# Kernel optimization log

Measured on AMD Instinct MI355X. Metric: run time of the kernel, lower is better.

## Reference

```python
import jax, jax.numpy as jnp
import numpy as np

NEG = -1000000.0  # same finite mask value as the Triton kernel


def setup_inputs() -> dict:
    key = jax.random.key(0)
    k1, k2, k3, k4 = jax.random.split(key, 4)
    B, H, KVH, S, D = 1, 32, 8, 2048, 128
    return {
        "q": jax.random.normal(k1, (B, H, S, D), dtype=jnp.float32),
        "k": jax.random.normal(k2, (B, KVH, S, D), dtype=jnp.float32),
        "v": jax.random.normal(k3, (B, KVH, S, D), dtype=jnp.float32),
        "sinks": jax.random.normal(k4, (H,), dtype=jnp.float32),
        "bandwidth": 1024,
    }


def reference(q, k, v, sinks, bandwidth):
    """Prefill flash attention with causal + sliding-window masking, GQA, and
    per-head attention sinks (extra logit in the softmax denominator)."""
    B, H, S, D = q.shape
    ratio = H // k.shape[1]  # KV_HEAD_RATIO
    kf = jnp.repeat(k, ratio, axis=1)  # [B,H,S,D]
    vf = jnp.repeat(v, ratio, axis=1)
    sm_scale = 1.0 / np.sqrt(D).astype(np.float32)

    logits = jnp.einsum("bhqd,bhkd->bhqk", q, kf) * sm_scale  # [B,H,S,S]
    q_pos = jnp.arange(S)[:, None]
    k_pos = jnp.arange(S)[None, :]
    mask = k_pos > q_pos  # causal
    if bandwidth > 0:
        mask = mask | (k_pos < q_pos - bandwidth + 1)  # sliding window
    logits = jnp.where(mask, NEG, logits)

    sink = sinks[None, :, None]  # [1,H,1] broadcast over batch, query
    m = jnp.maximum(jnp.max(logits, axis=-1), sink)  # [B,H,S]
    p = jnp.exp(logits - m[..., None])
    denom = p.sum(axis=-1) + jnp.exp(sink - m)  # sink contributes to denom only
    out = jnp.einsum("bhqk,bhkd->bhqd", p, vf) / denom[..., None]
    return out
```

## Files before the change

### kernel.cpp

```cpp
#include <hip/hip_runtime.h>
#include <hip/hip_bf16.h>

typedef __bf16 bf16x8 __attribute__((ext_vector_type(8)));
typedef unsigned short u16x8 __attribute__((ext_vector_type(8)));
typedef unsigned int u32x4 __attribute__((ext_vector_type(4)));
typedef float f32x4 __attribute__((ext_vector_type(4)));

#define SLEN 2048
#define DDIM 128
#define NH   32
#define NKVH 8
#define QBLK 64
#define KVB  32
#define KPAD 136
#define VPAD 40
#define PW2  20
#define MINIT  -1e30f
#define MASKED -3e30f

static __device__ __forceinline__ unsigned short f2bfu(float f) {
  union { float f; unsigned u; } x; x.f = f;
  return (unsigned short)((x.u + 0x7fffu + ((x.u >> 16) & 1u)) >> 16);
}
static __device__ __forceinline__ float bfu2f(unsigned short u) {
  union { unsigned u; float f; } x; x.u = ((unsigned)u) << 16;
  return x.f;
}
static __device__ __forceinline__ unsigned cvt_pk_bf16(float lo, float hi) {
  unsigned r;
  asm("v_cvt_pk_bf16_f32 %0, %1, %2" : "=v"(r) : "v"(lo), "v"(hi));
  return r;
}
static __device__ __forceinline__ f32x4 mfma_bf16(u16x8 a, u16x8 b, f32x4 c) {
  return __builtin_amdgcn_mfma_f32_16x16x32_bf16(
      __builtin_bit_cast(bf16x8, a), __builtin_bit_cast(bf16x8, b), c, 0, 0, 0);
}

__global__ __launch_bounds__(256) void conv_kv(const float* __restrict__ k,
                                               const float* __restrict__ v,
                                               unsigned* __restrict__ kdst,
                                               unsigned short* __restrict__ vt) {
  __shared__ unsigned T32[32][17];
  const int bb = blockIdx.x;
  if (bb < 1024) {
    const int i = bb * 256 + threadIdx.x;
    const float4 f0 = ((const float4*)k)[2 * i];
    const float4 f1 = ((const float4*)k)[2 * i + 1];
    u32x4 o = { cvt_pk_bf16(f0.x, f0.y), cvt_pk_bf16(f0.z, f0.w),
                cvt_pk_bf16(f1.x, f1.y), cvt_pk_bf16(f1.z, f1.w) };
    ((u32x4*)kdst)[i] = o;
    return;
  }
  const int b   = bb - 1024;
  const int dt  = b & 3;
  const int st  = (b >> 2) & 63;
  const int kvh = b >> 8;
  const int r  = threadIdx.x >> 3;
  const int cg = threadIdx.x & 7;
  const float4 f = *(const float4*)(v + ((size_t)(kvh * SLEN + st * 32 + r) * DDIM) + dt * 32 + cg * 4);
  T32[r][cg * 2]     = cvt_pk_bf16(f.x, f.y);
  T32[r][cg * 2 + 1] = cvt_pk_bf16(f.z, f.w);
  __syncthreads();
  const int dr = threadIdx.x >> 3;
  const unsigned sel = (dr & 1) ? 0x07060302u : 0x05040100u;
  const unsigned a0 = T32[cg * 4 + 0][dr >> 1], a1 = T32[cg * 4 + 1][dr >> 1];
  const unsigned a2 = T32[cg * 4 + 2][dr >> 1], a3 = T32[cg * 4 + 3][dr >> 1];
  unsigned short* vp = vt + (size_t)kvh * DDIM * SLEN + (size_t)(dt * 32 + dr) * SLEN + st * 32 + cg * 4;
  const unsigned w0 = __builtin_amdgcn_perm(a1, a0, sel);
  const unsigned w1 = __builtin_amdgcn_perm(a3, a2, sel);
  vp[0] = (unsigned short)(w0 & 0xffff);
  vp[1] = (unsigned short)(w0 >> 16);
  vp[2] = (unsigned short)(w1 & 0xffff);
  vp[3] = (unsigned short)(w1 >> 16);
}

__global__ __launch_bounds__(256, 4) void attn_fwd(
    const float* __restrict__ q, const unsigned short* __restrict__ kbf,
    const unsigned short* __restrict__ vtg, const float* __restrict__ sinks,
    const int* __restrict__ bwp, float* __restrict__ out,
    unsigned short* __restrict__ pO, float* __restrict__ pm,
    float* __restrict__ pl, const int nch) {
  __shared__ unsigned short Kl[KVB][KPAD];
  __shared__ unsigned short Vt[DDIM][VPAD];
  __shared__ unsigned Pex[4][16][PW2];
  __shared__ float SmS[4][16];

  const int tid  = threadIdx.x;
  const int wid  = tid >> 6;
  const int lane = tid & 63;
  const int ln   = lane & 15;
  const int hi   = lane >> 4;

  const int B   = blockIdx.x;
  const int x   = B & 7;
  const int j   = B >> 3;
  const int per = 4 * nch;
  const int qt  = 31 - (j / per);
  const int rem = j % per;
  const int hh  = (nch == 2) ? (rem >> 1) : rem;
  const int c   = (nch == 2) ? (rem & 1) : 0;
  const int h   = x * 4 + hh;
  const int kvh = x;
  const int q0  = qt * QBLK;
  const int qrow0 = q0 + wid * 16;
  const int qpos  = qrow0 + ln;

  const int bwv    = bwp[0];
  const int lo_off = (bwv > 0) ? (bwv - 1) : SLEN;

  const int T0 = max(0, q0 - lo_off) >> 5;
  const int T1 = (q0 + QBLK - 1) >> 5;
  const int N  = T1 - T0 + 1;
  const int ch = (N + nch - 1) / nch;
  const int Ts = T0 + c * ch;
  const int Te = min(T1, Ts + ch - 1);

  const float sm_scale = 0.08838834764831845f;

  u16x8 qf[4];
  {
    const float* qp = q + ((size_t)(h * SLEN + qpos) * DDIM) + hi * 8;
    #pragma unroll
    for (int dk = 0; dk < 4; ++dk) {
      float4 f0 = *(const float4*)(qp + dk * 32);
      float4 f1 = *(const float4*)(qp + dk * 32 + 4);
      u32x4 t = { cvt_pk_bf16(f0.x, f0.y), cvt_pk_bf16(f0.z, f0.w),
                  cvt_pk_bf16(f1.x, f1.y), cvt_pk_bf16(f1.z, f1.w) };
      qf[dk] = __builtin_bit_cast(u16x8, t);
    }
  }

  float m_ln = MINIT, l_ln = 0.0f;
  f32x4 oacc[8];
  #pragma unroll
  for (int nt = 0; nt < 8; ++nt) oacc[nt] = f32x4{0.f, 0.f, 0.f, 0.f};

  const unsigned short* Kg = kbf + (size_t)kvh * SLEN * DDIM;
  const unsigned short* Vg = vtg + (size_t)kvh * DDIM * SLEN;

  const int kr0 = tid >> 4,          kc0 = (tid & 15) * 8;
  const int kr1 = (256 + tid) >> 4;
  const int vr0 = tid >> 2,          vc0 = (tid & 3) * 8;
  const int vr1 = (256 + tid) >> 2;

  const int kbS = Ts * 32, kbE = Te * 32;

  u16x8 pk0, pk1, pv0, pv1;
  {
    pk0 = *(const u16x8*)(Kg + (size_t)(kbS + kr0) * DDIM + kc0);
    pk1 = *(const u16x8*)(Kg + (size_t)(kbS + kr1) * DDIM + kc0);
    pv0 = *(const u16x8*)(Vg + (size_t)vr0 * SLEN + kbS + vc0);
    pv1 = *(const u16x8*)(Vg + (size_t)vr1 * SLEN + kbS + vc0);
  }

  for (int kb = kbS; kb <= kbE; kb += KVB) {
    __syncthreads();
    *(u16x8*)&Kl[kr0][kc0] = pk0;
    *(u16x8*)&Kl[kr1][kc0] = pk1;
    *(u16x8*)&Vt[vr0][vc0] = pv0;
    *(u16x8*)&Vt[vr1][vc0] = pv1;
    __syncthreads();

    {
      const int nb = min(kb + KVB, kbE);
      pk0 = *(const u16x8*)(Kg + (size_t)(nb + kr0) * DDIM + kc0);
      pk1 = *(const u16x8*)(Kg + (size_t)(nb + kr1) * DDIM + kc0);
      pv0 = *(const u16x8*)(Vg + (size_t)vr0 * SLEN + nb + vc0);
      pv1 = *(const u16x8*)(Vg + (size_t)vr1 * SLEN + nb + vc0);
    }

    if (kb > qrow0 + 15) continue;
    if (kb + KVB - 1 < qrow0 - lo_off) continue;

    f32x4 sacc0 = {0,0,0,0}, sacc1 = {0,0,0,0};
    #pragma unroll
    for (int dk = 0; dk < 4; ++dk)
      sacc0 = mfma_bf16(*(const u16x8*)&Kl[ln][dk*32 + hi*8], qf[dk], sacc0);
    #pragma unroll
    for (int dk = 0; dk < 4; ++dk)
      sacc1 = mfma_bf16(*(const u16x8*)&Kl[16 + ln][dk*32 + hi*8], qf[dk], sacc1);

    float p[8];
    #pragma unroll
    for (int r = 0; r < 4; ++r) {
      const int kp0 = kb + hi * 4 + r;
      const int kp1 = kp0 + 16;
      const bool ok0 = (kp0 <= qpos) && (kp0 >= qpos - lo_off);
      const bool ok1 = (kp1 <= qpos) && (kp1 >= qpos - lo_off);
      p[r]     = ok0 ? sacc0[r] * sm_scale : MASKED;
      p[4 + r] = ok1 ? sacc1[r] * sm_scale : MASKED;
    }

    float mx = fmaxf(fmaxf(fmaxf(p[0], p[1]), fmaxf(p[2], p[3])),
                     fmaxf(fmaxf(p[4], p[5]), fmaxf(p[6], p[7])));
    mx = fmaxf(mx, __shfl_xor(mx, 16));
    mx = fmaxf(mx, __shfl_xor(mx, 32));

    if (__any(mx > m_ln + 8.0f)) {
      const float mn   = fmaxf(m_ln, mx);
      const float corr = __expf(m_ln - mn);
      l_ln *= corr;
      m_ln = mn;
      if (hi == 0) SmS[wid][ln] = corr;
      float corr4[4];
      #pragma unroll
      for (int r = 0; r < 4; ++r) corr4[r] = SmS[wid][hi * 4 + r];
      #pragma unroll
      for (int nt = 0; nt < 8; ++nt)
        #pragma unroll
        for (int r = 0; r < 4; ++r) oacc[nt][r] *= corr4[r];
    }

    float s = 0.0f;
    #pragma unroll
    for (int jj = 0; jj < 8; ++jj) { p[jj] = __expf(p[jj] - m_ln); s += p[jj]; }
    s += __shfl_xor(s, 16);
    s += __shfl_xor(s, 32);
    l_ln += s;

    Pex[wid][ln][hi * 2]         = cvt_pk_bf16(p[0], p[1]);
    Pex[wid][ln][hi * 2 + 1]     = cvt_pk_bf16(p[2], p[3]);
    Pex[wid][ln][8 + hi * 2]     = cvt_pk_bf16(p[4], p[5]);
    Pex[wid][ln][8 + hi * 2 + 1] = cvt_pk_bf16(p[6], p[7]);
    const u32x4 paw = *(const u32x4*)&Pex[wid][ln][hi * 4];
    const u16x8 pa  = __builtin_bit_cast(u16x8, paw);

    #pragma unroll
    for (int nt = 0; nt < 8; ++nt) {
      const u16x8 vb = *(const u16x8*)&Vt[nt*16 + ln][hi*8];
      oacc[nt] = mfma_bf16(pa, vb, oacc[nt]);
    }
  }

  if (nch == 1) {
    const float sink = sinks[h];
    const float M  = fmaxf(m_ln, sink);
    const float ed = __expf(m_ln - M);
    const float fac_ln = ed / (l_ln * ed + __expf(sink - M));
    if (hi == 0) SmS[wid][ln] = fac_ln;
    float fac4[4];
    #pragma unroll
    for (int r = 0; r < 4; ++r) fac4[r] = SmS[wid][hi * 4 + r];
    #pragma unroll
    for (int r = 0; r < 4; ++r) {
      float* op = out + ((size_t)(h * SLEN + qrow0 + hi*4 + r) * DDIM) + ln;
      #pragma unroll
      for (int nt = 0; nt < 8; ++nt) op[nt * 16] = oacc[nt][r] * fac4[r];
    }
  } else {
    const size_t Lb = ((size_t)(h * 32 + qt)) * 2 + c;
    if (hi == 0) {
      pm[Lb * 64 + wid * 16 + ln] = m_ln;
      pl[Lb * 64 + wid * 16 + ln] = l_ln;
    }
    #pragma unroll
    for (int r = 0; r < 4; ++r) {
      unsigned short* po = pO + (Lb * 64 + wid * 16 + hi * 4 + r) * 128 + ln;
      #pragma unroll
      for (int nt = 0; nt < 8; ++nt) po[nt * 16] = f2bfu(oacc[nt][r]);
    }
  }
}

__global__ __launch_bounds__(256) void merge2(
    const unsigned short* __restrict__ pO, const float* __restrict__ pm,
    const float* __restrict__ pl, const float* __restrict__ sinks,
    float* __restrict__ out) {
  const int blk = blockIdx.x;
  const int h   = blk >> 5;
  const int row = threadIdx.x >> 2;
  const int d0  = (threadIdx.x & 3) * 32;
  const size_t b0 = (size_t)blk * 2, b1 = b0 + 1;
  const float m0 = pm[b0 * 64 + row], l0 = pl[b0 * 64 + row];
  const float m1 = pm[b1 * 64 + row], l1 = pl[b1 * 64 + row];
  const float sink = sinks[h];
  const float M  = fmaxf(fmaxf(m0, m1), sink);
  const float e0 = __expf(m0 - M), e1 = __expf(m1 - M);
  const float inv = 1.0f / (l0 * e0 + l1 * e1 + __expf(sink - M));
  const float s0 = e0 * inv, s1 = e1 * inv;
  const unsigned short* p0 = pO + (b0 * 64 + row) * 128 + d0;
  const unsigned short* p1 = pO + (b1 * 64 + row) * 128 + d0;
  float* op = out + ((size_t)blk * 64 + row) * 128 + d0;
  #pragma unroll
  for (int i = 0; i < 4; ++i) {
    u16x8 a = *(const u16x8*)(p0 + i * 8);
    u16x8 b = *(const u16x8*)(p1 + i * 8);
    float4 o0, o1;
    o0.x = bfu2f(a[0]) * s0 + bfu2f(b[0]) * s1;
    o0.y = bfu2f(a[1]) * s0 + bfu2f(b[1]) * s1;
    o0.z = bfu2f(a[2]) * s0 + bfu2f(b[2]) * s1;
    o0.w = bfu2f(a[3]) * s0 + bfu2f(b[3]) * s1;
    o1.x = bfu2f(a[4]) * s0 + bfu2f(b[4]) * s1;
    o1.y = bfu2f(a[5]) * s0 + bfu2f(b[5]) * s1;
    o1.z = bfu2f(a[6]) * s0 + bfu2f(b[6]) * s1;
    o1.w = bfu2f(a[7]) * s0 + bfu2f(b[7]) * s1;
    *(float4*)(op + i * 8)     = o0;
    *(float4*)(op + i * 8 + 4) = o1;
  }
}

extern "C" void kernel_launch(void* const* d_in, const int* in_sizes, int n_in,
                              void* d_out, int out_size, void* d_ws, size_t ws_size,
                              hipStream_t stream) {
  const float* q     = (const float*)d_in[0];
  const float* k     = (const float*)d_in[1];
  const float* v     = (const float*)d_in[2];
  const float* sinks = (const float*)d_in[3];
  const int*   bw    = (const int*)d_in[4];
  float* out = (float*)d_out;

  const size_t kvBytes = (size_t)NKVH * SLEN * DDIM * 2;
  unsigned short* kbf = (unsigned short*)d_ws;
  unsigned short* vtg = kbf + (size_t)NKVH * SLEN * DDIM;

  const size_t nPart   = (size_t)2048 * 64;
  const size_t oBytes  = nPart * 128 * 2;
  const size_t mlBytes = nPart * 4 * 2;
  const size_t need2   = 2 * kvBytes + oBytes + mlBytes;

  const int nch = (ws_size >= need2) ? 2 : 1;

  unsigned short* pO = vtg + (size_t)NKVH * SLEN * DDIM;
  float* pm = (float*)((char*)pO + oBytes);
  float* pl = pm + nPart;

  conv_kv<<<dim3(1024 + NKVH * 64 * 4), 256, 0, stream>>>(k, v, (unsigned*)kbf, vtg);
  attn_fwd<<<dim3(1024 * nch), 256, 0, stream>>>(q, kbf, vtg, sinks, bw, out,
                                                 pO, pm, pl, nch);
  if (nch == 2)
    merge2<<<dim3(1024), 256, 0, stream>>>(pO, pm, pl, sinks, out);
}
```

Measured before the change: 79.77 us.

## Double query tile to 128 rows so each wave reuses K/V fragments across two groups

Each block now processes 128 query rows, with each wave handling two 16-row groups that share the same K and V fragments read from LDS. This halves the K/V global and LDS traffic per query row and the number of blocks, and the partial-result layout and merge indexing are rewritten to match. In exchange, each thread holds twice the accumulators, so register pressure rises and the launch bound drops to 3 blocks per SM. There are also fewer blocks overall, which can hurt load balance across CUs.

```diff
diff --git a/kernel.cpp b/kernel.cpp
--- a/kernel.cpp
+++ b/kernel.cpp
@@ -10,7 +10,7 @@
 #define DDIM 128
 #define NH   32
 #define NKVH 8
-#define QBLK 64
+#define QBLK 128
 #define KVB  32
 #define KPAD 136
 #define VPAD 40
@@ -74,7 +74,7 @@
   vp[3] = (unsigned short)(w1 >> 16);
 }
 
-__global__ __launch_bounds__(256, 4) void attn_fwd(
+__global__ __launch_bounds__(256, 3) void attn_fwd(
     const float* __restrict__ q, const unsigned short* __restrict__ kbf,
     const unsigned short* __restrict__ vtg, const float* __restrict__ sinks,
     const int* __restrict__ bwp, float* __restrict__ out,
@@ -82,8 +82,8 @@
     float* __restrict__ pl, const int nch) {
   __shared__ unsigned short Kl[KVB][KPAD];
   __shared__ unsigned short Vt[DDIM][VPAD];
-  __shared__ unsigned Pex[4][16][PW2];
-  __shared__ float SmS[4][16];
+  __shared__ unsigned Pex[4][2][16][PW2];
+  __shared__ float SmS[4][2][16];
 
   const int tid  = threadIdx.x;
   const int wid  = tid >> 6;
@@ -95,15 +95,14 @@
   const int x   = B & 7;
   const int j   = B >> 3;
   const int per = 4 * nch;
-  const int qt  = 31 - (j / per);
+  const int qt  = 15 - (j / per);
   const int rem = j % per;
   const int hh  = (nch == 2) ? (rem >> 1) : rem;
   const int c   = (nch == 2) ? (rem & 1) : 0;
   const int h   = x * 4 + hh;
   const int kvh = x;
   const int q0  = qt * QBLK;
-  const int qrow0 = q0 + wid * 16;
-  const int qpos  = qrow0 + ln;
+  const int qrow0 = q0 + wid * 32;
 
   const int bwv    = bwp[0];
   const int lo_off = (bwv > 0) ? (bwv - 1) : SLEN;
@@ -117,23 +116,26 @@
 
   const float sm_scale = 0.08838834764831845f;
 
-  u16x8 qf[4];
-  {
-    const float* qp = q + ((size_t)(h * SLEN + qpos) * DDIM) + hi * 8;
+  u16x8 qf[2][4];
+  #pragma unroll
+  for (int g = 0; g < 2; ++g) {
+    const float* qp = q + ((size_t)(h * SLEN + qrow0 + g * 16 + ln) * DDIM) + hi * 8;
     #pragma unroll
     for (int dk = 0; dk < 4; ++dk) {
       float4 f0 = *(const float4*)(qp + dk * 32);
       float4 f1 = *(const float4*)(qp + dk * 32 + 4);
       u32x4 t = { cvt_pk_bf16(f0.x, f0.y), cvt_pk_bf16(f0.z, f0.w),
                   cvt_pk_bf16(f1.x, f1.y), cvt_pk_bf16(f1.z, f1.w) };
-      qf[dk] = __builtin_bit_cast(u16x8, t);
-    }
-  }
-
-  float m_ln = MINIT, l_ln = 0.0f;
-  f32x4 oacc[8];
+      qf[g][dk] = __builtin_bit_cast(u16x8, t);
+    }
+  }
+
+  float m[2] = {MINIT, MINIT}, l[2] = {0.0f, 0.0f};
+  f32x4 oacc[2][8];
   #pragma unroll
-  for (int nt = 0; nt < 8; ++nt) oacc[nt] = f32x4{0.f, 0.f, 0.f, 0.f};
+  for (int g = 0; g < 2; ++g)
+    #pragma unroll
+    for (int nt = 0; nt < 8; ++nt) oacc[g][nt] = f32x4{0.f, 0.f, 0.f, 0.f};
 
   const unsigned short* Kg = kbf + (size_t)kvh * SLEN * DDIM;
   const unsigned short* Vg = vtg + (size_t)kvh * DDIM * SLEN;
@@ -169,95 +171,119 @@
       pv1 = *(const u16x8*)(Vg + (size_t)vr1 * SLEN + nb + vc0);
     }
 
-    if (kb > qrow0 + 15) continue;
+    if (kb > qrow0 + 31) continue;
     if (kb + KVB - 1 < qrow0 - lo_off) continue;
 
-    f32x4 sacc0 = {0,0,0,0}, sacc1 = {0,0,0,0};
-    #pragma unroll
-    for (int dk = 0; dk < 4; ++dk)
-      sacc0 = mfma_bf16(*(const u16x8*)&Kl[ln][dk*32 + hi*8], qf[dk], sacc0);
-    #pragma unroll
-    for (int dk = 0; dk < 4; ++dk)
-      sacc1 = mfma_bf16(*(const u16x8*)&Kl[16 + ln][dk*32 + hi*8], qf[dk], sacc1);
-
-    float p[8];
+    f32x4 s00 = {0,0,0,0}, s01 = {0,0,0,0};
+    f32x4 s10 = {0,0,0,0}, s11 = {0,0,0,0};
+    #pragma unroll
+    for (int dk = 0; dk < 4; ++dk) {
+      const u16x8 kf = *(const u16x8*)&Kl[ln][dk*32 + hi*8];
+      s00 = mfma_bf16(kf, qf[0][dk], s00);
+      s01 = mfma_bf16(kf, qf[1][dk], s01);
+    }
+    #pragma unroll
+    for (int dk = 0; dk < 4; ++dk) {
+      const u16x8 kf = *(const u16x8*)&Kl[16 + ln][dk*32 + hi*8];
+      s10 = mfma_bf16(kf, qf[0][dk], s10);
+      s11 = mfma_bf16(kf, qf[1][dk], s11);
+    }
+
+    float p0[8], p1[8];
+    const int qpos0 = qrow0 + ln, qpos1 = qrow0 + 16 + ln;
     #pragma unroll
     for (int r = 0; r < 4; ++r) {
       const int kp0 = kb + hi * 4 + r;
       const int kp1 = kp0 + 16;
-      const bool ok0 = (kp0 <= qpos) && (kp0 >= qpos - lo_off);
-      const bool ok1 = (kp1 <= qpos) && (kp1 >= qpos - lo_off);
-      p[r]     = ok0 ? sacc0[r] * sm_scale : MASKED;
-      p[4 + r] = ok1 ? sacc1[r] * sm_scale : MASKED;
-    }
-
-    float mx = fmaxf(fmaxf(fmaxf(p[0], p[1]), fmaxf(p[2], p[3])),
-                     fmaxf(fmaxf(p[4], p[5]), fmaxf(p[6], p[7])));
-    mx = fmaxf(mx, __shfl_xor(mx, 16));
-    mx = fmaxf(mx, __shfl_xor(mx, 32));
-
-    if (__any(mx > m_ln + 8.0f)) {
-      const float mn   = fmaxf(m_ln, mx);
-      const float corr = __expf(m_ln - mn);
-      l_ln *= corr;
-      m_ln = mn;
-      if (hi == 0) SmS[wid][ln] = corr;
-      float corr4[4];
-      #pragma unroll
-      for (int r = 0; r < 4; ++r) corr4[r] = SmS[wid][hi * 4 + r];
+      p0[r]     = ((kp0 <= qpos0) && (kp0 >= qpos0 - lo_off)) ? s00[r] * sm_scale : MASKED;
+      p0[4 + r] = ((kp1 <= qpos0) && (kp1 >= qpos0 - lo_off)) ? s10[r] * sm_scale : MASKED;
+      p1[r]     = ((kp0 <= qpos1) && (kp0 >= qpos1 - lo_off)) ? s01[r] * sm_scale : MASKED;
+      p1[4 + r] = ((kp1 <= qpos1) && (kp1 >= qpos1 - lo_off)) ? s11[r] * sm_scale : MASKED;
+    }
+
+    float mx0 = fmaxf(fmaxf(fmaxf(p0[0], p0[1]), fmaxf(p0[2], p0[3])),
+                      fmaxf(fmaxf(p0[4], p0[5]), fmaxf(p0[6], p0[7])));
+    float mx1 = fmaxf(fmaxf(fmaxf(p1[0], p1[1]), fmaxf(p1[2], p1[3])),
+                      fmaxf(fmaxf(p1[4], p1[5]), fmaxf(p1[6], p1[7])));
+    mx0 = fmaxf(mx0, __shfl_xor(mx0, 16));
+    mx0 = fmaxf(mx0, __shfl_xor(mx0, 32));
+    mx1 = fmaxf(mx1, __shfl_xor(mx1, 16));
+    mx1 = fmaxf(mx1, __shfl_xor(mx1, 32));
+
+    if (__any((mx0 > m[0] + 8.0f) || (mx1 > m[1] + 8.0f))) {
+      const float mn0 = fmaxf(m[0], mx0), mn1 = fmaxf(m[1], mx1);
+      const float c0 = __expf(m[0] - mn0), c1 = __expf(m[1] - mn1);
+      l[0] *= c0; l[1] *= c1; m[0] = mn0; m[1] = mn1;
+      if (hi == 0) { SmS[wid][0][ln] = c0; SmS[wid][1][ln] = c1; }
+      float c40[4], c41[4];
+      #pragma unroll
+      for (int r = 0; r < 4; ++r) { c40[r] = SmS[wid][0][hi*4 + r]; c41[r] = SmS[wid][1][hi*4 + r]; }
       #pragma unroll
       for (int nt = 0; nt < 8; ++nt)
         #pragma unroll
-        for (int r = 0; r < 4; ++r) oacc[nt][r] *= corr4[r];
-    }
-
-    float s = 0.0f;
-    #pragma unroll
-    for (int jj = 0; jj < 8; ++jj) { p[jj] = __expf(p[jj] - m_ln); s += p[jj]; }
-    s += __shfl_xor(s, 16);
-    s += __shfl_xor(s, 32);
-    l_ln += s;
-
-    Pex[wid][ln][hi * 2]         = cvt_pk_bf16(p[0], p[1]);
-    Pex[wid][ln][hi * 2 + 1]     = cvt_pk_bf16(p[2], p[3]);
-    Pex[wid][ln][8 + hi * 2]     = cvt_pk_bf16(p[4], p[5]);
-    Pex[wid][ln][8 + hi * 2 + 1] = cvt_pk_bf16(p[6], p[7]);
-    const u32x4 paw = *(const u32x4*)&Pex[wid][ln][hi * 4];
-    const u16x8 pa  = __builtin_bit_cast(u16x8, paw);
+        for (int r = 0; r < 4; ++r) { oacc[0][nt][r] *= c40[r]; oacc[1][nt][r] *= c41[r]; }
+    }
+
+    float s0 = 0.0f, s1 = 0.0f;
+    #pragma unroll
+    for (int jj = 0; jj < 8; ++jj) {
+      p0[jj] = __expf(p0[jj] - m[0]); s0 += p0[jj];
+      p1[jj] = __expf(p1[jj] - m[1]); s1 += p1[jj];
+    }
+    s0 += __shfl_xor(s0, 16); s0 += __shfl_xor(s0, 32); l[0] += s0;
+    s1 += __shfl_xor(s1, 16); s1 += __shfl_xor(s1, 32); l[1] += s1;
+
+    Pex[wid][0][ln][hi * 2]         = cvt_pk_bf16(p0[0], p0[1]);
+    Pex[wid][0][ln][hi * 2 + 1]     = cvt_pk_bf16(p0[2], p0[3]);
+    Pex[wid][0][ln][8 + hi * 2]     = cvt_pk_bf16(p0[4], p0[5]);
+    Pex[wid][0][ln][8 + hi * 2 + 1] = cvt_pk_bf16(p0[6], p0[7]);
+    Pex[wid][1][ln][hi * 2]         = cvt_pk_bf16(p1[0], p1[1]);
+    Pex[wid][1][ln][hi * 2 + 1]     = cvt_pk_bf16(p1[2], p1[3]);
+    Pex[wid][1][ln][8 + hi * 2]     = cvt_pk_bf16(p1[4], p1[5]);
+    Pex[wid][1][ln][8 + hi * 2 + 1] = cvt_pk_bf16(p1[6], p1[7]);
+    const u16x8 pa0 = __builtin_bit_cast(u16x8, *(const u32x4*)&Pex[wid][0][ln][hi * 4]);
+    const u16x8 pa1 = __builtin_bit_cast(u16x8, *(const u32x4*)&Pex[wid][1][ln][hi * 4]);
 
     #pragma unroll
     for (int nt = 0; nt < 8; ++nt) {
       const u16x8 vb = *(const u16x8*)&Vt[nt*16 + ln][hi*8];
-      oacc[nt] = mfma_bf16(pa, vb, oacc[nt]);
+      oacc[0][nt] = mfma_bf16(pa0, vb, oacc[0][nt]);
+      oacc[1][nt] = mfma_bf16(pa1, vb, oacc[1][nt]);
     }
   }
 
   if (nch == 1) {
     const float sink = sinks[h];
-    const float M  = fmaxf(m_ln, sink);
-    const float ed = __expf(m_ln - M);
-    const float fac_ln = ed / (l_ln * ed + __expf(sink - M));
-    if (hi == 0) SmS[wid][ln] = fac_ln;
-    float fac4[4];
-    #pragma unroll
-    for (int r = 0; r < 4; ++r) fac4[r] = SmS[wid][hi * 4 + r];
-    #pragma unroll
-    for (int r = 0; r < 4; ++r) {
-      float* op = out + ((size_t)(h * SLEN + qrow0 + hi*4 + r) * DDIM) + ln;
-      #pragma unroll
-      for (int nt = 0; nt < 8; ++nt) op[nt * 16] = oacc[nt][r] * fac4[r];
+    #pragma unroll
+    for (int g = 0; g < 2; ++g) {
+      const float M  = fmaxf(m[g], sink);
+      const float ed = __expf(m[g] - M);
+      const float fac_ln = ed / (l[g] * ed + __expf(sink - M));
+      if (hi == 0) SmS[wid][g][ln] = fac_ln;
+      float fac4[4];
+      #pragma unroll
+      for (int r = 0; r < 4; ++r) fac4[r] = SmS[wid][g][hi * 4 + r];
+      #pragma unroll
+      for (int r = 0; r < 4; ++r) {
+        float* op = out + ((size_t)(h * SLEN + qrow0 + g*16 + hi*4 + r) * DDIM) + ln;
+        #pragma unroll
+        for (int nt = 0; nt < 8; ++nt) op[nt * 16] = oacc[g][nt][r] * fac4[r];
+      }
     }
   } else {
-    const size_t Lb = ((size_t)(h * 32 + qt)) * 2 + c;
-    if (hi == 0) {
-      pm[Lb * 64 + wid * 16 + ln] = m_ln;
-      pl[Lb * 64 + wid * 16 + ln] = l_ln;
-    }
-    #pragma unroll
-    for (int r = 0; r < 4; ++r) {
-      unsigned short* po = pO + (Lb * 64 + wid * 16 + hi * 4 + r) * 128 + ln;
-      #pragma unroll
-      for (int nt = 0; nt < 8; ++nt) po[nt * 16] = f2bfu(oacc[nt][r]);
+    const size_t Lb = ((size_t)(h * 16 + qt)) * 2 + c;
+    #pragma unroll
+    for (int g = 0; g < 2; ++g) {
+      if (hi == 0) {
+        pm[Lb * 128 + wid * 32 + g * 16 + ln] = m[g];
+        pl[Lb * 128 + wid * 32 + g * 16 + ln] = l[g];
+      }
+      #pragma unroll
+      for (int r = 0; r < 4; ++r) {
+        unsigned short* po = pO + (Lb * 128 + wid * 32 + g * 16 + hi * 4 + r) * 128 + ln;
+        #pragma unroll
+        for (int nt = 0; nt < 8; ++nt) po[nt * 16] = f2bfu(oacc[g][nt][r]);
+      }
     }
   }
 }
@@ -266,21 +292,24 @@
     const unsigned short* __restrict__ pO, const float* __restrict__ pm,
     const float* __restrict__ pl, const float* __restrict__ sinks,
     float* __restrict__ out) {
-  const int blk = blockIdx.x;
-  const int h   = blk >> 5;
-  const int row = threadIdx.x >> 2;
-  const int d0  = (threadIdx.x & 3) * 32;
-  const size_t b0 = (size_t)blk * 2, b1 = b0 + 1;
-  const float m0 = pm[b0 * 64 + row], l0 = pl[b0 * 64 + row];
-  const float m1 = pm[b1 * 64 + row], l1 = pl[b1 * 64 + row];
+  const int blk  = blockIdx.x;
+  const int h    = blk >> 5;
+  const int rloc = (blk & 31) * 64 + (threadIdx.x >> 2);
+  const int d0   = (threadIdx.x & 3) * 32;
+  const int qt   = rloc >> 7;
+  const int lr   = rloc & 127;
+  const size_t r0 = ((size_t)((h * 16 + qt) * 2 + 0)) * 128 + lr;
+  const size_t r1 = r0 + 128;
+  const float m0 = pm[r0], l0 = pl[r0];
+  const float m1 = pm[r1], l1 = pl[r1];
   const float sink = sinks[h];
   const float M  = fmaxf(fmaxf(m0, m1), sink);
   const float e0 = __expf(m0 - M), e1 = __expf(m1 - M);
   const float inv = 1.0f / (l0 * e0 + l1 * e1 + __expf(sink - M));
   const float s0 = e0 * inv, s1 = e1 * inv;
-  const unsigned short* p0 = pO + (b0 * 64 + row) * 128 + d0;
-  const unsigned short* p1 = pO + (b1 * 64 + row) * 128 + d0;
-  float* op = out + ((size_t)blk * 64 + row) * 128 + d0;
+  const unsigned short* p0 = pO + r0 * 128 + d0;
+  const unsigned short* p1 = pO + r1 * 128 + d0;
+  float* op = out + ((size_t)h * SLEN + rloc) * DDIM + d0;
   #pragma unroll
   for (int i = 0; i < 4; ++i) {
     u16x8 a = *(const u16x8*)(p0 + i * 8);
@@ -313,7 +342,7 @@
   unsigned short* kbf = (unsigned short*)d_ws;
   unsigned short* vtg = kbf + (size_t)NKVH * SLEN * DDIM;
 
-  const size_t nPart   = (size_t)2048 * 64;
+  const size_t nPart   = (size_t)NH * 16 * 2 * 128;
   const size_t oBytes  = nPart * 128 * 2;
   const size_t mlBytes = nPart * 4 * 2;
   const size_t need2   = 2 * kvBytes + oBytes + mlBytes;
@@ -325,8 +354,8 @@
   float* pl = pm + nPart;
 
   conv_kv<<<dim3(1024 + NKVH * 64 * 4), 256, 0, stream>>>(k, v, (unsigned*)kbf, vtg);
-  attn_fwd<<<dim3(1024 * nch), 256, 0, stream>>>(q, kbf, vtg, sinks, bw, out,
-                                                 pO, pm, pl, nch);
+  attn_fwd<<<dim3(512 * nch), 256, 0, stream>>>(q, kbf, vtg, sinks, bw, out,
+                                                pO, pm, pl, nch);
   if (nch == 2)
     merge2<<<dim3(1024), 256, 0, stream>>>(pO, pm, pl, sinks, out);
 }
```

Result: slower. 86.84 us (+8.9%).

## Double-buffer K/V tiles in LDS via direct global-to-LDS loads with XOR swizzle

Applied to the files above, without the earlier changes.

Replaces the register-staged K/V prefetch (global load into registers, then store to padded LDS between two barriers) with direct global_load_lds into double-buffered LDS tiles. An XOR swizzle replaces the padding to avoid bank conflicts, and each iteration needs only one barrier. The kernel is templated on chunk count and the merge is generalized. This is meant to cut register pressure and LDS store traffic and to overlap loads with compute. In exchange it doubles LDS use per block, which may reduce occupancy, and it relies on the ordering semantics of the async LDS loads.

```diff
diff --git a/kernel.cpp b/kernel.cpp
--- a/kernel.cpp
+++ b/kernel.cpp
@@ -10,11 +10,7 @@
 #define DDIM 128
 #define NH   32
 #define NKVH 8
-#define QBLK 64
 #define KVB  32
-#define KPAD 136
-#define VPAD 40
-#define PW2  20
 #define MINIT  -1e30f
 #define MASKED -3e30f
 
@@ -34,6 +30,11 @@
 static __device__ __forceinline__ f32x4 mfma_bf16(u16x8 a, u16x8 b, f32x4 c) {
   return __builtin_amdgcn_mfma_f32_16x16x32_bf16(
       __builtin_bit_cast(bf16x8, a), __builtin_bit_cast(bf16x8, b), c, 0, 0, 0);
+}
+static __device__ __forceinline__ void gload16(const unsigned short* g, unsigned short* l) {
+  __builtin_amdgcn_global_load_lds(
+      (const __attribute__((address_space(1))) unsigned*)g,
+      (__attribute__((address_space(3))) unsigned*)l, 16, 0, 0);
 }
 
 __global__ __launch_bounds__(256) void conv_kv(const float* __restrict__ k,
@@ -74,15 +75,17 @@
   vp[3] = (unsigned short)(w1 >> 16);
 }
 
+template <int NCH>
 __global__ __launch_bounds__(256, 4) void attn_fwd(
     const float* __restrict__ q, const unsigned short* __restrict__ kbf,
     const unsigned short* __restrict__ vtg, const float* __restrict__ sinks,
     const int* __restrict__ bwp, float* __restrict__ out,
     unsigned short* __restrict__ pO, float* __restrict__ pm,
-    float* __restrict__ pl, const int nch) {
-  __shared__ unsigned short Kl[KVB][KPAD];
-  __shared__ unsigned short Vt[DDIM][VPAD];
-  __shared__ unsigned Pex[4][16][PW2];
+    float* __restrict__ pl) {
+  constexpr int NQT = 32;
+  __shared__ unsigned short KB[2][KVB][DDIM];
+  __shared__ unsigned short VB[2][DDIM][KVB];
+  __shared__ unsigned Pex[4][16][16];
   __shared__ float SmS[4][16];
 
   const int tid  = threadIdx.x;
@@ -94,14 +97,14 @@
   const int B   = blockIdx.x;
   const int x   = B & 7;
   const int j   = B >> 3;
-  const int per = 4 * nch;
-  const int qt  = 31 - (j / per);
+  constexpr int per = 4 * NCH;
+  const int qt  = NQT - 1 - (j / per);
   const int rem = j % per;
-  const int hh  = (nch == 2) ? (rem >> 1) : rem;
-  const int c   = (nch == 2) ? (rem & 1) : 0;
+  const int hh  = rem / NCH;
+  const int c   = rem % NCH;
   const int h   = x * 4 + hh;
   const int kvh = x;
-  const int q0  = qt * QBLK;
+  const int q0  = qt * 64;
   const int qrow0 = q0 + wid * 16;
   const int qpos  = qrow0 + ln;
 
@@ -109,9 +112,9 @@
   const int lo_off = (bwv > 0) ? (bwv - 1) : SLEN;
 
   const int T0 = max(0, q0 - lo_off) >> 5;
-  const int T1 = (q0 + QBLK - 1) >> 5;
+  const int T1 = (q0 + 63) >> 5;
   const int N  = T1 - T0 + 1;
-  const int ch = (N + nch - 1) / nch;
+  const int ch = (N + NCH - 1) / NCH;
   const int Ts = T0 + c * ch;
   const int Te = min(T1, Ts + ch - 1);
 
@@ -138,101 +141,109 @@
   const unsigned short* Kg = kbf + (size_t)kvh * SLEN * DDIM;
   const unsigned short* Vg = vtg + (size_t)kvh * DDIM * SLEN;
 
-  const int kr0 = tid >> 4,          kc0 = (tid & 15) * 8;
-  const int kr1 = (256 + tid) >> 4;
-  const int vr0 = tid >> 2,          vc0 = (tid & 3) * 8;
-  const int vr1 = (256 + tid) >> 2;
-
-  const int kbS = Ts * 32, kbE = Te * 32;
-
-  u16x8 pk0, pk1, pv0, pv1;
-  {
-    pk0 = *(const u16x8*)(Kg + (size_t)(kbS + kr0) * DDIM + kc0);
-    pk1 = *(const u16x8*)(Kg + (size_t)(kbS + kr1) * DDIM + kc0);
-    pv0 = *(const u16x8*)(Vg + (size_t)vr0 * SLEN + kbS + vc0);
-    pv1 = *(const u16x8*)(Vg + (size_t)vr1 * SLEN + kbS + vc0);
-  }
-
-  for (int kb = kbS; kb <= kbE; kb += KVB) {
-    __syncthreads();
-    *(u16x8*)&Kl[kr0][kc0] = pk0;
-    *(u16x8*)&Kl[kr1][kc0] = pk1;
-    *(u16x8*)&Vt[vr0][vc0] = pv0;
-    *(u16x8*)&Vt[vr1][vc0] = pv1;
-    __syncthreads();
+  int koff[2], voff[2];
+  #pragma unroll
+  for (int c2 = 0; c2 < 2; ++c2) {
+    const int r = wid * 8 + c2 * 4 + (lane >> 4);
+    koff[c2] = r * DDIM + (((lane & 15) ^ (r & 7)) * 8);
+    const int d = wid * 32 + c2 * 16 + (lane >> 2);
+    voff[c2] = d * SLEN + (((lane & 3) ^ ((lane >> 3) & 3)) * 8);
+  }
+
+  int kfo[4];
+  #pragma unroll
+  for (int dk = 0; dk < 4; ++dk)
+    kfo[dk] = ln * DDIM + (((dk * 4 + hi) ^ (ln & 7)) * 8);
+  const int vswz = (hi ^ ((ln >> 1) & 3)) * 8;
+
+  if (Ts <= Te) {
+    const int kbS = Ts * 32, kbE = Te * 32;
 
     {
-      const int nb = min(kb + KVB, kbE);
-      pk0 = *(const u16x8*)(Kg + (size_t)(nb + kr0) * DDIM + kc0);
-      pk1 = *(const u16x8*)(Kg + (size_t)(nb + kr1) * DDIM + kc0);
-      pv0 = *(const u16x8*)(Vg + (size_t)vr0 * SLEN + nb + vc0);
-      pv1 = *(const u16x8*)(Vg + (size_t)vr1 * SLEN + nb + vc0);
-    }
-
-    if (kb > qrow0 + 15) continue;
-    if (kb + KVB - 1 < qrow0 - lo_off) continue;
-
-    f32x4 sacc0 = {0,0,0,0}, sacc1 = {0,0,0,0};
-    #pragma unroll
-    for (int dk = 0; dk < 4; ++dk)
-      sacc0 = mfma_bf16(*(const u16x8*)&Kl[ln][dk*32 + hi*8], qf[dk], sacc0);
-    #pragma unroll
-    for (int dk = 0; dk < 4; ++dk)
-      sacc1 = mfma_bf16(*(const u16x8*)&Kl[16 + ln][dk*32 + hi*8], qf[dk], sacc1);
-
-    float p[8];
-    #pragma unroll
-    for (int r = 0; r < 4; ++r) {
-      const int kp0 = kb + hi * 4 + r;
-      const int kp1 = kp0 + 16;
-      const bool ok0 = (kp0 <= qpos) && (kp0 >= qpos - lo_off);
-      const bool ok1 = (kp1 <= qpos) && (kp1 >= qpos - lo_off);
-      p[r]     = ok0 ? sacc0[r] * sm_scale : MASKED;
-      p[4 + r] = ok1 ? sacc1[r] * sm_scale : MASKED;
-    }
-
-    float mx = fmaxf(fmaxf(fmaxf(p[0], p[1]), fmaxf(p[2], p[3])),
-                     fmaxf(fmaxf(p[4], p[5]), fmaxf(p[6], p[7])));
-    mx = fmaxf(mx, __shfl_xor(mx, 16));
-    mx = fmaxf(mx, __shfl_xor(mx, 32));
-
-    if (__any(mx > m_ln + 8.0f)) {
-      const float mn   = fmaxf(m_ln, mx);
-      const float corr = __expf(m_ln - mn);
-      l_ln *= corr;
-      m_ln = mn;
-      if (hi == 0) SmS[wid][ln] = corr;
-      float corr4[4];
-      #pragma unroll
-      for (int r = 0; r < 4; ++r) corr4[r] = SmS[wid][hi * 4 + r];
-      #pragma unroll
-      for (int nt = 0; nt < 8; ++nt)
+      gload16(Kg + (size_t)kbS * DDIM + koff[0], &KB[0][wid * 8][0]);
+      gload16(Kg + (size_t)kbS * DDIM + koff[1], &KB[0][wid * 8 + 4][0]);
+      gload16(Vg + (size_t)kbS + voff[0], &VB[0][wid * 32][0]);
+      gload16(Vg + (size_t)kbS + voff[1], &VB[0][wid * 32 + 16][0]);
+    }
+
+    int cur = 0;
+    for (int kb = kbS; kb <= kbE; kb += KVB) {
+      __syncthreads();
+
+      if (kb + KVB <= kbE) {
+        const int nb = kb + KVB;
+        const int nxt = cur ^ 1;
+        gload16(Kg + (size_t)nb * DDIM + koff[0], &KB[nxt][wid * 8][0]);
+        gload16(Kg + (size_t)nb * DDIM + koff[1], &KB[nxt][wid * 8 + 4][0]);
+        gload16(Vg + (size_t)nb + voff[0], &VB[nxt][wid * 32][0]);
+        gload16(Vg + (size_t)nb + voff[1], &VB[nxt][wid * 32 + 16][0]);
+      }
+
+      const bool skip = (kb > qrow0 + 15) || (kb + KVB - 1 < qrow0 - lo_off);
+      if (!skip) {
+        const unsigned short* kbp = &KB[cur][0][0];
+        const unsigned short* vbp = &VB[cur][0][0];
+
+        f32x4 sacc0 = {0,0,0,0}, sacc1 = {0,0,0,0};
         #pragma unroll
-        for (int r = 0; r < 4; ++r) oacc[nt][r] *= corr4[r];
-    }
-
-    float s = 0.0f;
-    #pragma unroll
-    for (int jj = 0; jj < 8; ++jj) { p[jj] = __expf(p[jj] - m_ln); s += p[jj]; }
-    s += __shfl_xor(s, 16);
-    s += __shfl_xor(s, 32);
-    l_ln += s;
-
-    Pex[wid][ln][hi * 2]         = cvt_pk_bf16(p[0], p[1]);
-    Pex[wid][ln][hi * 2 + 1]     = cvt_pk_bf16(p[2], p[3]);
-    Pex[wid][ln][8 + hi * 2]     = cvt_pk_bf16(p[4], p[5]);
-    Pex[wid][ln][8 + hi * 2 + 1] = cvt_pk_bf16(p[6], p[7]);
-    const u32x4 paw = *(const u32x4*)&Pex[wid][ln][hi * 4];
-    const u16x8 pa  = __builtin_bit_cast(u16x8, paw);
-
-    #pragma unroll
-    for (int nt = 0; nt < 8; ++nt) {
-      const u16x8 vb = *(const u16x8*)&Vt[nt*16 + ln][hi*8];
-      oacc[nt] = mfma_bf16(pa, vb, oacc[nt]);
-    }
-  }
-
-  if (nch == 1) {
+        for (int dk = 0; dk < 4; ++dk) {
+          sacc0 = mfma_bf16(*(const u16x8*)(kbp + kfo[dk]), qf[dk], sacc0);
+          sacc1 = mfma_bf16(*(const u16x8*)(kbp + kfo[dk] + 16 * DDIM), qf[dk], sacc1);
+        }
+
+        float p[8];
+        #pragma unroll
+        for (int r = 0; r < 4; ++r) {
+          const int kp0 = kb + hi * 4 + r;
+          const int kp1 = kp0 + 16;
+          p[r]     = ((kp0 <= qpos) && (kp0 >= qpos - lo_off)) ? sacc0[r] * sm_scale : MASKED;
+          p[4 + r] = ((kp1 <= qpos) && (kp1 >= qpos - lo_off)) ? sacc1[r] * sm_scale : MASKED;
+        }
+
+        float mx = fmaxf(fmaxf(fmaxf(p[0], p[1]), fmaxf(p[2], p[3])),
+                         fmaxf(fmaxf(p[4], p[5]), fmaxf(p[6], p[7])));
+        mx = fmaxf(mx, __shfl_xor(mx, 16));
+        mx = fmaxf(mx, __shfl_xor(mx, 32));
+
+        if (__any(mx > m_ln + 8.0f)) {
+          const float mn   = fmaxf(m_ln, mx);
+          const float corr = __expf(m_ln - mn);
+          l_ln *= corr;
+          m_ln = mn;
+          if (hi == 0) SmS[wid][ln] = corr;
+          float c4[4];
+          #pragma unroll
+          for (int r = 0; r < 4; ++r) c4[r] = SmS[wid][hi * 4 + r];
+          #pragma unroll
+          for (int nt = 0; nt < 8; ++nt)
+            #pragma unroll
+            for (int r = 0; r < 4; ++r) oacc[nt][r] *= c4[r];
+        }
+
+        float s = 0.0f;
+        #pragma unroll
+        for (int jj = 0; jj < 8; ++jj) { p[jj] = __expf(p[jj] - m_ln); s += p[jj]; }
+        s += __shfl_xor(s, 16);
+        s += __shfl_xor(s, 32);
+        l_ln += s;
+
+        Pex[wid][ln][hi * 2]         = cvt_pk_bf16(p[0], p[1]);
+        Pex[wid][ln][hi * 2 + 1]     = cvt_pk_bf16(p[2], p[3]);
+        Pex[wid][ln][8 + hi * 2]     = cvt_pk_bf16(p[4], p[5]);
+        Pex[wid][ln][8 + hi * 2 + 1] = cvt_pk_bf16(p[6], p[7]);
+        const u16x8 pa = __builtin_bit_cast(u16x8, *(const u32x4*)&Pex[wid][ln][hi * 4]);
+
+        #pragma unroll
+        for (int nt = 0; nt < 8; ++nt) {
+          const u16x8 vb = *(const u16x8*)(vbp + (nt * 16 + ln) * KVB + vswz);
+          oacc[nt] = mfma_bf16(pa, vb, oacc[nt]);
+        }
+      }
+      cur ^= 1;
+    }
+  }
+
+  if (NCH == 1) {
     const float sink = sinks[h];
     const float M  = fmaxf(m_ln, sink);
     const float ed = __expf(m_ln - M);
@@ -248,7 +259,7 @@
       for (int nt = 0; nt < 8; ++nt) op[nt * 16] = oacc[nt][r] * fac4[r];
     }
   } else {
-    const size_t Lb = ((size_t)(h * 32 + qt)) * 2 + c;
+    const size_t Lb = ((size_t)(h * NQT + qt)) * NCH + c;
     if (hi == 0) {
       pm[Lb * 64 + wid * 16 + ln] = m_ln;
       pl[Lb * 64 + wid * 16 + ln] = l_ln;
@@ -262,41 +273,51 @@
   }
 }
 
-__global__ __launch_bounds__(256) void merge2(
+template <int NCH, int QBLK, int NQT>
+__global__ __launch_bounds__(256) void mergeN(
     const unsigned short* __restrict__ pO, const float* __restrict__ pm,
     const float* __restrict__ pl, const float* __restrict__ sinks,
     float* __restrict__ out) {
-  const int blk = blockIdx.x;
-  const int h   = blk >> 5;
-  const int row = threadIdx.x >> 2;
-  const int d0  = (threadIdx.x & 3) * 32;
-  const size_t b0 = (size_t)blk * 2, b1 = b0 + 1;
-  const float m0 = pm[b0 * 64 + row], l0 = pl[b0 * 64 + row];
-  const float m1 = pm[b1 * 64 + row], l1 = pl[b1 * 64 + row];
+  const int t    = blockIdx.x * 256 + threadIdx.x;
+  const int rid  = t >> 2;
+  const int d0   = (t & 3) * 32;
+  const int h    = rid >> 11;
+  const int qpos = rid & 2047;
+  const int qt   = qpos / QBLK;
+  const int lr   = qpos % QBLK;
+  const size_t base = ((size_t)(h * NQT + qt) * NCH) * QBLK + lr;
   const float sink = sinks[h];
-  const float M  = fmaxf(fmaxf(m0, m1), sink);
-  const float e0 = __expf(m0 - M), e1 = __expf(m1 - M);
-  const float inv = 1.0f / (l0 * e0 + l1 * e1 + __expf(sink - M));
-  const float s0 = e0 * inv, s1 = e1 * inv;
-  const unsigned short* p0 = pO + (b0 * 64 + row) * 128 + d0;
-  const unsigned short* p1 = pO + (b1 * 64 + row) * 128 + d0;
-  float* op = out + ((size_t)blk * 64 + row) * 128 + d0;
-  #pragma unroll
-  for (int i = 0; i < 4; ++i) {
-    u16x8 a = *(const u16x8*)(p0 + i * 8);
-    u16x8 b = *(const u16x8*)(p1 + i * 8);
-    float4 o0, o1;
-    o0.x = bfu2f(a[0]) * s0 + bfu2f(b[0]) * s1;
-    o0.y = bfu2f(a[1]) * s0 + bfu2f(b[1]) * s1;
-    o0.z = bfu2f(a[2]) * s0 + bfu2f(b[2]) * s1;
-    o0.w = bfu2f(a[3]) * s0 + bfu2f(b[3]) * s1;
-    o1.x = bfu2f(a[4]) * s0 + bfu2f(b[4]) * s1;
-    o1.y = bfu2f(a[5]) * s0 + bfu2f(b[5]) * s1;
-    o1.z = bfu2f(a[6]) * s0 + bfu2f(b[6]) * s1;
-    o1.w = bfu2f(a[7]) * s0 + bfu2f(b[7]) * s1;
-    *(float4*)(op + i * 8)     = o0;
-    *(float4*)(op + i * 8 + 4) = o1;
-  }
+  float mc[NCH], lc[NCH];
+  float M = sink;
+  #pragma unroll
+  for (int c = 0; c < NCH; ++c) {
+    mc[c] = pm[base + (size_t)c * QBLK];
+    lc[c] = pl[base + (size_t)c * QBLK];
+    M = fmaxf(M, mc[c]);
+  }
+  float denom = __expf(sink - M);
+  float sc[NCH];
+  #pragma unroll
+  for (int c = 0; c < NCH; ++c) { sc[c] = __expf(mc[c] - M); denom += lc[c] * sc[c]; }
+  const float inv = 1.0f / denom;
+  float o[32];
+  #pragma unroll
+  for (int i = 0; i < 32; ++i) o[i] = 0.f;
+  #pragma unroll
+  for (int c = 0; c < NCH; ++c) {
+    const unsigned short* pp = pO + (base + (size_t)c * QBLK) * 128 + d0;
+    const float s = sc[c] * inv;
+    #pragma unroll
+    for (int i = 0; i < 4; ++i) {
+      u16x8 a = *(const u16x8*)(pp + i * 8);
+      #pragma unroll
+      for (int jj = 0; jj < 8; ++jj) o[i*8+jj] += bfu2f(a[jj]) * s;
+    }
+  }
+  float* op = out + (size_t)rid * 128 + d0;
+  #pragma unroll
+  for (int i = 0; i < 8; ++i)
+    *(float4*)(op + i*4) = make_float4(o[i*4], o[i*4+1], o[i*4+2], o[i*4+3]);
 }
 
 extern "C" void kernel_launch(void* const* d_in, const int* in_sizes, int n_in,
@@ -309,24 +330,22 @@
   const int*   bw    = (const int*)d_in[4];
   float* out = (float*)d_out;
 
-  const size_t kvBytes = (size_t)NKVH * SLEN * DDIM * 2;
+  const size_t kvElems = (size_t)NKVH * SLEN * DDIM;
   unsigned short* kbf = (unsigned short*)d_ws;
-  unsigned short* vtg = kbf + (size_t)NKVH * SLEN * DDIM;
-
-  const size_t nPart   = (size_t)2048 * 64;
-  const size_t oBytes  = nPart * 128 * 2;
-  const size_t mlBytes = nPart * 4 * 2;
-  const size_t need2   = 2 * kvBytes + oBytes + mlBytes;
-
-  const int nch = (ws_size >= need2) ? 2 : 1;
-
-  unsigned short* pO = vtg + (size_t)NKVH * SLEN * DDIM;
-  float* pm = (float*)((char*)pO + oBytes);
-  float* pl = pm + nPart;
+  unsigned short* vtg = kbf + kvElems;
+  unsigned short* pO  = vtg + kvElems;
+
+  const size_t nPart2 = (size_t)NH * 32 * 2 * 64;
+  const size_t need2  = 4 * kvElems + nPart2 * 128 * 2 + nPart2 * 8;
 
   conv_kv<<<dim3(1024 + NKVH * 64 * 4), 256, 0, stream>>>(k, v, (unsigned*)kbf, vtg);
-  attn_fwd<<<dim3(1024 * nch), 256, 0, stream>>>(q, kbf, vtg, sinks, bw, out,
-                                                 pO, pm, pl, nch);
-  if (nch == 2)
-    merge2<<<dim3(1024), 256, 0, stream>>>(pO, pm, pl, sinks, out);
-}
+
+  if (ws_size >= need2) {
+    float* pm = (float*)(pO + nPart2 * 128);
+    float* pl = pm + nPart2;
+    attn_fwd<2><<<dim3(2048), 256, 0, stream>>>(q, kbf, vtg, sinks, bw, out, pO, pm, pl);
+    mergeN<2, 64, 32><<<dim3(1024), 256, 0, stream>>>(pO, pm, pl, sinks, out);
+  } else {
+    attn_fwd<1><<<dim3(1024), 256, 0, stream>>>(q, kbf, vtg, sinks, bw, out, pO, nullptr, nullptr);
+  }
+}
```

After: 85.83 us. 1.08x slower.
